# Kernel tuning notes

Hardware: AMD Instinct MI355X
Metric: run time of the kernel (lower is better)

Reference implementation:

```python
import jax, jax.numpy as jnp
import numpy as np

H = 256          # hidden_dim
B = 64           # molecules
M = 64           # atoms per molecule (equal-size molecules)
N = B * M        # total nodes
NE = 119         # element classes
NB = 5           # bond classes
EPS = 1e-5
OFF_I, OFF_J = np.where(~np.eye(M, dtype=bool))  # static off-diagonal pair order (i-major, j!=i)


def _gelu(x):
    return jax.nn.gelu(x, approximate=False)


def _ln(x, g, b):
    mu = jnp.mean(x, axis=-1, keepdims=True)
    var = jnp.mean((x - mu) ** 2, axis=-1, keepdims=True)
    return (x - mu) * jax.lax.rsqrt(var + EPS) * g + b


def _mlp(x, W1, b1, g, bn, W2, b2, W3, b3):
    x = _gelu(x @ W1 + b1)
    x = _ln(x, g, bn)
    x = _gelu(x @ W2 + b2)
    return x @ W3 + b3


def setup_inputs():
    key = jax.random.key(0)
    ks = jax.random.split(key, 16)
    s = 0.02
    def lin(k, fi, fo):
        return jax.random.normal(k, (fi, fo), jnp.float32) * s
    inp = {}
    inp["h"] = jax.random.normal(ks[0], (N, H), jnp.float32)
    inp["pos"] = jax.random.normal(ks[1], (N, 3), jnp.float32) * 3.0
    inp["edge_index"] = jax.random.randint(ks[2], (2, N * 8), 0, N)
    inp["batch"] = jnp.repeat(jnp.arange(B), M)
    # atom_predictor params
    inp["aW1"] = lin(ks[3], H, H); inp["ab1"] = jnp.zeros((H,))
    inp["ag"] = jnp.ones((H,)); inp["abn"] = jnp.zeros((H,))
    inp["aW2"] = lin(ks[4], H, H // 2); inp["ab2"] = jnp.zeros((H // 2,))
    inp["aW3"] = lin(ks[5], H // 2, NE); inp["ab3"] = jnp.zeros((NE,))
    # valency_predictor params
    inp["vW1"] = lin(ks[6], H + NE, H); inp["vb1"] = jnp.zeros((H,))
    inp["vg"] = jnp.ones((H,)); inp["vbn"] = jnp.zeros((H,))
    inp["vW2"] = lin(ks[7], H, H // 2); inp["vb2"] = jnp.zeros((H // 2,))
    inp["vW3"] = lin(ks[8], H // 2, 1); inp["vb3"] = jnp.zeros((1,))
    # bond_predictor params
    inp["bW1"] = lin(ks[9], 2 * H + 4, H); inp["bb1"] = jnp.zeros((H,))
    inp["bg"] = jnp.ones((H,)); inp["bbn"] = jnp.zeros((H,))
    inp["bW2"] = lin(ks[10], H, H // 2); inp["bb2"] = jnp.zeros((H // 2,))
    inp["bW3"] = lin(ks[11], H // 2, NB); inp["bb3"] = jnp.zeros((NB,))
    # chemical constant buffers (stand-ins for RDKit tables)
    mv = np.ones(NE, np.float32) * 4.0
    mv[[1, 9, 17, 35, 53]] = 1.0; mv[8] = 2.0; mv[7] = 3.0; mv[16] = 6.0; mv[15] = 5.0
    inp["max_valences"] = jnp.asarray(mv)
    cr = np.ones(NE, np.float32) * 1.5
    cr[1] = 0.31; cr[6] = 0.76; cr[7] = 0.71; cr[8] = 0.66; cr[9] = 0.57; cr[16] = 1.05
    inp["covalent_radii"] = jnp.asarray(cr)
    return inp


def _forward(h, pos, aW1, ab1, ag, abn, aW2, ab2, aW3, ab3,
             vW1, vb1, vg, vbn, vW2, vb2, vW3, vb3,
             bW1, bb1, bg, bbn, bW2, bb2, bW3, bb3,
             max_valences, covalent_radii):
    atom_logits = _mlp(h, aW1, ab1, ag, abn, aW2, ab2, aW3, ab3)        # [N,119]
    atom_probs = jax.nn.softmax(atom_logits, axis=-1)
    val = _mlp(jnp.concatenate([h, atom_probs], -1), vW1, vb1, vg, vbn, vW2, vb2, vW3, vb3)
    val = jax.nn.softplus(val)                                          # [N,1]
    pred = jnp.clip(jnp.argmax(atom_probs, -1), 0, 118)
    max_allowed = max_valences[pred]                                    # [N]
    # torch.min([N], [N,1]) broadcasts to [N,N] in the original -- reproduced faithfully
    valency_constrained = jnp.minimum(val[:, 0], max_allowed[:, None])  # [N,N]
    # vectorized pairwise bond prediction per molecule (equal-size molecules)
    hB = h.reshape(B, M, H)
    pB = pos.reshape(B, M, 3)
    probsB = atom_probs.reshape(B, M, NE)
    dist = jnp.linalg.norm(pB[:, :, None, :] - pB[:, None, :, :], axis=-1)  # [B,M,M]
    radii = covalent_radii[jnp.minimum(jnp.argmax(probsB, -1), 118)]        # [B,M]
    expected = radii[:, :, None] + radii[:, None, :]                        # [B,M,M]
    close = (dist < 3.0).astype(h.dtype)
    feats = jnp.concatenate([
        jnp.broadcast_to(hB[:, :, None, :], (B, M, M, H)),
        jnp.broadcast_to(hB[:, None, :, :], (B, M, M, H)),
        dist[..., None], expected[..., None],
        (dist / expected)[..., None], close[..., None],
    ], axis=-1)                                                             # [B,M,M,2H+4]
    logits = _mlp(feats, bW1, bb1, bg, bbn, bW2, bb2, bW3, bb3)             # [B,M,M,5]
    probs5 = jax.nn.softmax(logits, axis=-1)
    e0 = jnp.zeros((NB,), h.dtype).at[0].set(1.0)
    diag = jnp.eye(M, dtype=bool)[None, :, :, None]
    adjacency = jnp.where(diag, e0, probs5)                                 # [B,M,M,5]
    bond_logits = logits[:, OFF_I, OFF_J, :].reshape(B * M * (M - 1), NB)   # skip i==j, i-major order
    return (atom_logits, bond_logits, valency_constrained, adjacency)


def reference(h, pos, edge_index, batch, aW1, ab1, ag, abn, aW2, ab2, aW3, ab3,
              vW1, vb1, vg, vbn, vW2, vb2, vW3, vb3,
              bW1, bb1, bg, bbn, bW2, bb2, bW3, bb3, max_valences, covalent_radii):
    # edge_index is unused by the original forward; batch is implicit in the [B,M] layout
    return _forward(h, pos, aW1, ab1, ag, abn, aW2, ab2, aW3, ab3,
                    vW1, vb1, vg, vbn, vW2, vb2, vW3, vb3,
                    bW1, bb1, bg, bbn, bW2, bb2, bW3, bb3,
                    max_valences, covalent_radii)
```

## Files before the change

kernel.cpp:

```cpp
#include <hip/hip_runtime.h>
#include <math.h>

#define NN   4096
#define HH   256
#define NEC  119
#define NBC  5
#define NMOL 64
#define MAT  64

#define OFF_ATOM   0
#define SZ_ATOM    (4096*119)
#define OFF_BOND   487424
#define SZ_BOND    (258048*5)
#define OFF_VALM   (487424+1290240)
#define SZ_VALM    (4096*4096)
#define OFF_ADJ    (1777664+16777216)

typedef short  bf16x8 __attribute__((ext_vector_type(8)));
typedef float  f32x4  __attribute__((ext_vector_type(4)));

__device__ __forceinline__ float gelu_f(float x) {
    float z = fabsf(x) * 0.70710678118654752f;
    float t = __builtin_amdgcn_rcpf(fmaf(0.3275911f, z, 1.0f));
    float p = t * fmaf(t, fmaf(t, fmaf(t, fmaf(t, 1.061405429f, -1.453152027f),
                                       1.421413741f), -0.284496736f), 0.254829592f);
    float er = fmaf(-p, __expf(-z * z), 1.0f);
    float s = copysignf(er, x);
    return 0.5f * x * (1.f + s);
}
__device__ __forceinline__ unsigned short f2bf(float x) {
    unsigned int u = __float_as_uint(x);
    unsigned int r = (u + 0x7fffu + ((u >> 16) & 1u)) >> 16;
    return (unsigned short)r;
}

__global__ __launch_bounds__(256) void k_front(
    const float* __restrict__ h,
    const float* __restrict__ aW1, const float* __restrict__ ab1,
    const float* __restrict__ ag,  const float* __restrict__ abn,
    const float* __restrict__ aW2, const float* __restrict__ ab2,
    const float* __restrict__ aW3, const float* __restrict__ ab3,
    const float* __restrict__ maxv, const float* __restrict__ covr,
    const float* __restrict__ vW1, const float* __restrict__ vb1,
    const float* __restrict__ vg,  const float* __restrict__ vbn,
    const float* __restrict__ vW2, const float* __restrict__ vb2,
    const float* __restrict__ vW3, const float* __restrict__ vb3,
    const float* __restrict__ bW1, const float* __restrict__ bb1,
    const float* __restrict__ bW2, const float* __restrict__ bW3,
    float* __restrict__ logits_out,
    float* __restrict__ ma, float* __restrict__ rad, float* __restrict__ val,
    float* __restrict__ P, float* __restrict__ Q,
    short* __restrict__ W2f, short* __restrict__ W3f)
{
    __shared__ float smem[7056];
    float (*hs)[376]   = (float(*)[376])smem;
    float (*z1)[256]   = (float(*)[256])(smem + 3008);
    float (*z2)[128]   = (float(*)[128])(smem + 5056);
    float (*llog)[120] = (float(*)[120])(smem + 6080);
    float (*redbuf)[2] = (float(*)[2])  (smem + 7040);

    const int t  = threadIdx.x;
    const int wv = t >> 6, ln = t & 63;

    if (blockIdx.x >= 512) {
        const int pb = blockIdx.x - 512;
        const int n0 = pb * 8;

        if (pb < 128) {
            const int id = pb * 256 + t;
            {
                const int e = id & 7, l = (id >> 3) & 63, ks = (id >> 9) & 7, ct = (id >> 12) & 7;
                const int k = ks * 32 + (l >> 4) * 8 + e;
                const int col = ct * 16 + (l & 15);
                W2f[id] = (short)f2bf(bW2[k * 128 + col]);
            }
            if (id < 2048) {
                const int e = id & 7, l = (id >> 3) & 63, ks = id >> 9;
                const int k = ks * 32 + (l >> 4) * 8 + e;
                const int col = l & 15;
                W3f[id] = (col < NBC) ? (short)f2bf(bW3[k * NBC + col]) : (short)0;
            }
        }

        float (*hq)[256] = (float(*)[256])smem;
        for (int idx = t; idx < 8 * 256; idx += 256)
            ((float*)hq)[idx] = h[(size_t)n0 * 256 + idx];
        __syncthreads();

        const int c = t;
        float accp[8], accq[8];
        float b1 = bb1[c];
        #pragma unroll
        for (int r = 0; r < 8; ++r) { accp[r] = b1; accq[r] = 0.f; }
        for (int k4 = 0; k4 < 64; ++k4) {
            const int k = k4 * 4;
            float p0 = bW1[(k + 0) * 256 + c];
            float p1 = bW1[(k + 1) * 256 + c];
            float p2 = bW1[(k + 2) * 256 + c];
            float p3 = bW1[(k + 3) * 256 + c];
            float q0 = bW1[(256 + k + 0) * 256 + c];
            float q1 = bW1[(256 + k + 1) * 256 + c];
            float q2 = bW1[(256 + k + 2) * 256 + c];
            float q3 = bW1[(256 + k + 3) * 256 + c];
            #pragma unroll
            for (int r = 0; r < 8; ++r) {
                float4 hv = *(const float4*)&hq[r][k];
                accp[r] = fmaf(hv.x, p0, accp[r]);
                accp[r] = fmaf(hv.y, p1, accp[r]);
                accp[r] = fmaf(hv.z, p2, accp[r]);
                accp[r] = fmaf(hv.w, p3, accp[r]);
                accq[r] = fmaf(hv.x, q0, accq[r]);
                accq[r] = fmaf(hv.y, q1, accq[r]);
                accq[r] = fmaf(hv.z, q2, accq[r]);
                accq[r] = fmaf(hv.w, q3, accq[r]);
            }
        }
        #pragma unroll
        for (int r = 0; r < 8; ++r) {
            P[(size_t)(n0 + r) * 256 + c] = accp[r];
            Q[(size_t)(n0 + r) * 256 + c] = accq[r];
        }
        return;
    }

    const int n0 = blockIdx.x * 8;

    for (int idx = t; idx < 8 * 256; idx += 256) {
        int r = idx >> 8, cc = idx & 255;
        hs[r][cc] = h[(size_t)(n0 + r) * 256 + cc];
    }
    if (t < 8) hs[t][375] = 0.f;
    __syncthreads();

    {
        const int c = t;
        float b1 = ab1[c];
        float acc[8];
        #pragma unroll
        for (int r = 0; r < 8; ++r) acc[r] = b1;
        for (int k4 = 0; k4 < 64; ++k4) {
            const int k = k4 * 4;
            float w0 = aW1[(k + 0) * 256 + c];
            float w1 = aW1[(k + 1) * 256 + c];
            float w2 = aW1[(k + 2) * 256 + c];
            float w3 = aW1[(k + 3) * 256 + c];
            #pragma unroll
            for (int r = 0; r < 8; ++r) {
                float4 hv = *(const float4*)&hs[r][k];
                acc[r] = fmaf(hv.x, w0, acc[r]);
                acc[r] = fmaf(hv.y, w1, acc[r]);
                acc[r] = fmaf(hv.z, w2, acc[r]);
                acc[r] = fmaf(hv.w, w3, acc[r]);
            }
        }
        #pragma unroll
        for (int r = 0; r < 8; ++r) z1[r][c] = gelu_f(acc[r]);
    }
    __syncthreads();

    for (int rr = 0; rr < 2; ++rr) {
        const int r = wv * 2 + rr;
        float s = 0.f, s2 = 0.f;
        #pragma unroll
        for (int q = 0; q < 4; ++q) {
            float v = z1[r][ln + q * 64];
            s += v; s2 = fmaf(v, v, s2);
        }
        #pragma unroll
        for (int m = 32; m >= 1; m >>= 1) {
            s  += __shfl_xor(s,  m, 64);
            s2 += __shfl_xor(s2, m, 64);
        }
        if (ln == 0) {
            float mu  = s * (1.f / 256.f);
            float var = s2 * (1.f / 256.f) - mu * mu;
            redbuf[r][0] = mu;
            redbuf[r][1] = rsqrtf(var + 1e-5f);
        }
    }
    __syncthreads();
    {
        const int c = t;
        float g = ag[c], b = abn[c];
        #pragma unroll
        for (int r = 0; r < 8; ++r)
            z1[r][c] = (z1[r][c] - redbuf[r][0]) * redbuf[r][1] * g + b;
    }
    __syncthreads();

    {
        const int c2 = t & 127, kh = t >> 7;
        float acc2[8];
        #pragma unroll
        for (int r = 0; r < 8; ++r) acc2[r] = 0.f;
        const int kb = kh * 128;
        for (int k4 = 0; k4 < 32; ++k4) {
            const int k = kb + k4 * 4;
            float w0 = aW2[(k + 0) * 128 + c2];
            float w1 = aW2[(k + 1) * 128 + c2];
            float w2 = aW2[(k + 2) * 128 + c2];
            float w3 = aW2[(k + 3) * 128 + c2];
            #pragma unroll
            for (int r = 0; r < 8; ++r) {
                float4 zv = *(const float4*)&z1[r][k];
                acc2[r] = fmaf(zv.x, w0, acc2[r]);
                acc2[r] = fmaf(zv.y, w1, acc2[r]);
                acc2[r] = fmaf(zv.z, w2, acc2[r]);
                acc2[r] = fmaf(zv.w, w3, acc2[r]);
            }
        }
        if (kh == 1) {
            #pragma unroll
            for (int r = 0; r < 8; ++r) z2[r][c2] = acc2[r];
        }
        __syncthreads();
        if (kh == 0) {
            float b2 = ab2[c2];
            #pragma unroll
            for (int r = 0; r < 8; ++r)
                z2[r][c2] = gelu_f(acc2[r] + z2[r][c2] + b2);
        }
    }
    __syncthreads();

    if (t < NEC) {
        const int c = t;
        float b3 = ab3[c];
        float acc3[8];
        #pragma unroll
        for (int r = 0; r < 8; ++r) acc3[r] = b3;
        for (int k4 = 0; k4 < 32; ++k4) {
            const int k = k4 * 4;
            float w0 = aW3[(k + 0) * NEC + c];
            float w1 = aW3[(k + 1) * NEC + c];
            float w2 = aW3[(k + 2) * NEC + c];
            float w3 = aW3[(k + 3) * NEC + c];
            #pragma unroll
            for (int r = 0; r < 8; ++r) {
                float4 zv = *(const float4*)&z2[r][k];
                acc3[r] = fmaf(zv.x, w0, acc3[r]);
                acc3[r] = fmaf(zv.y, w1, acc3[r]);
                acc3[r] = fmaf(zv.z, w2, acc3[r]);
                acc3[r] = fmaf(zv.w, w3, acc3[r]);
            }
        }
        #pragma unroll
        for (int r = 0; r < 8; ++r) {
            llog[r][c] = acc3[r];
            logits_out[(size_t)(n0 + r) * NEC + c] = acc3[r];
        }
    }
    __syncthreads();

    for (int rr = 0; rr < 2; ++rr) {
        const int r = wv * 2 + rr;
        float v1 = llog[r][ln];
        float v2 = (ln + 64 < NEC) ? llog[r][ln + 64] : -1e30f;
        float mx; int mi;
        if (v2 > v1) { mx = v2; mi = ln + 64; } else { mx = v1; mi = ln; }
        #pragma unroll
        for (int m = 32; m >= 1; m >>= 1) {
            float ov = __shfl_xor(mx, m, 64);
            int   oi = __shfl_xor(mi, m, 64);
            if (ov > mx || (ov == mx && oi < mi)) { mx = ov; mi = oi; }
        }
        float e1 = __expf(v1 - mx);
        float e2 = (ln + 64 < NEC) ? __expf(v2 - mx) : 0.f;
        float s = e1 + e2;
        #pragma unroll
        for (int m = 32; m >= 1; m >>= 1) s += __shfl_xor(s, m, 64);
        float inv = __builtin_amdgcn_rcpf(s);
        hs[r][256 + ln] = e1 * inv;
        if (ln + 64 < NEC) hs[r][256 + ln + 64] = e2 * inv;
        if (ln == 0) {
            ma[n0 + r]  = maxv[mi];
            rad[n0 + r] = covr[mi];
        }
    }
    __syncthreads();

    {
        const int c = t;
        float b1 = vb1[c];
        float acc[8];
        #pragma unroll
        for (int r = 0; r < 8; ++r) acc[r] = b1;
        for (int k4 = 0; k4 < 93; ++k4) {
            const int k = k4 * 4;
            float w0 = vW1[(k + 0) * 256 + c];
            float w1 = vW1[(k + 1) * 256 + c];
            float w2 = vW1[(k + 2) * 256 + c];
            float w3 = vW1[(k + 3) * 256 + c];
            #pragma unroll
            for (int r = 0; r < 8; ++r) {
                float4 hv = *(const float4*)&hs[r][k];
                acc[r] = fmaf(hv.x, w0, acc[r]);
                acc[r] = fmaf(hv.y, w1, acc[r]);
                acc[r] = fmaf(hv.z, w2, acc[r]);
                acc[r] = fmaf(hv.w, w3, acc[r]);
            }
        }
        {
            float w0 = vW1[372 * 256 + c];
            float w1 = vW1[373 * 256 + c];
            float w2 = vW1[374 * 256 + c];
            #pragma unroll
            for (int r = 0; r < 8; ++r) {
                acc[r] = fmaf(hs[r][372], w0, acc[r]);
                acc[r] = fmaf(hs[r][373], w1, acc[r]);
                acc[r] = fmaf(hs[r][374], w2, acc[r]);
            }
        }
        #pragma unroll
        for (int r = 0; r < 8; ++r) z1[r][c] = gelu_f(acc[r]);
    }
    __syncthreads();

    for (int rr = 0; rr < 2; ++rr) {
        const int r = wv * 2 + rr;
        float s = 0.f, s2 = 0.f;
        #pragma unroll
        for (int q = 0; q < 4; ++q) {
            float v = z1[r][ln + q * 64];
            s += v; s2 = fmaf(v, v, s2);
        }
        #pragma unroll
        for (int m = 32; m >= 1; m >>= 1) {
            s  += __shfl_xor(s,  m, 64);
            s2 += __shfl_xor(s2, m, 64);
        }
        if (ln == 0) {
            float mu  = s * (1.f / 256.f);
            float var = s2 * (1.f / 256.f) - mu * mu;
            redbuf[r][0] = mu;
            redbuf[r][1] = rsqrtf(var + 1e-5f);
        }
    }
    __syncthreads();
    {
        const int c = t;
        float g = vg[c], b = vbn[c];
        #pragma unroll
        for (int r = 0; r < 8; ++r)
            z1[r][c] = (z1[r][c] - redbuf[r][0]) * redbuf[r][1] * g + b;
    }
    __syncthreads();

    {
        const int c2 = t & 127, kh = t >> 7;
        float acc2[8];
        #pragma unroll
        for (int r = 0; r < 8; ++r) acc2[r] = 0.f;
        const int kb = kh * 128;
        for (int k4 = 0; k4 < 32; ++k4) {
            const int k = kb + k4 * 4;
            float w0 = vW2[(k + 0) * 128 + c2];
            float w1 = vW2[(k + 1) * 128 + c2];
            float w2 = vW2[(k + 2) * 128 + c2];
            float w3 = vW2[(k + 3) * 128 + c2];
            #pragma unroll
            for (int r = 0; r < 8; ++r) {
                float4 zv = *(const float4*)&z1[r][k];
                acc2[r] = fmaf(zv.x, w0, acc2[r]);
                acc2[r] = fmaf(zv.y, w1, acc2[r]);
                acc2[r] = fmaf(zv.z, w2, acc2[r]);
                acc2[r] = fmaf(zv.w, w3, acc2[r]);
            }
        }
        if (kh == 1) {
            #pragma unroll
            for (int r = 0; r < 8; ++r) z2[r][c2] = acc2[r];
        }
        __syncthreads();
        if (kh == 0) {
            float b2 = vb2[c2];
            #pragma unroll
            for (int r = 0; r < 8; ++r)
                z2[r][c2] = gelu_f(acc2[r] + z2[r][c2] + b2);
        }
    }
    __syncthreads();

    for (int rr = 0; rr < 2; ++rr) {
        const int r = wv * 2 + rr;
        float p = fmaf(z2[r][ln], vW3[ln], z2[r][ln + 64] * vW3[ln + 64]);
        #pragma unroll
        for (int m = 32; m >= 1; m >>= 1) p += __shfl_xor(p, m, 64);
        if (ln == 0) {
            float x = p + vb3[0];
            val[n0 + r] = (x > 15.f) ? x : log1pf(expf(x));
        }
    }
}

__global__ __launch_bounds__(256) void k_back(
    const float* __restrict__ pos, const float* __restrict__ rad,
    const float* __restrict__ P, const float* __restrict__ Q,
    const float* __restrict__ bW1,
    const float* __restrict__ bg, const float* __restrict__ bbn,
    const float* __restrict__ bb2,
    const short* __restrict__ W2f, const short* __restrict__ W3f,
    const float* __restrict__ bb3,
    const float* __restrict__ val, const float* __restrict__ ma,
    float* __restrict__ bond_logits, float* __restrict__ adjacency,
    float* __restrict__ valmat)
{
    __shared__ float posr[64][4];
    __shared__ float bb2s[128];
    __shared__ unsigned short Xs[64 * 256];
    __shared__ float Ls[64][5];
    unsigned short* Ys = Xs;

    const int t  = threadIdx.x;

    if (blockIdx.x >= 4096) {
        const int i0 = (blockIdx.x - 4096) * 8;
        const float4* v4 = (const float4*)val;
        for (int rr = 0; rr < 8; ++rr) {
            const int i = i0 + rr;
            const float mi = ma[i];
            float4* o4 = (float4*)(valmat + (size_t)i * 4096);
            for (int j = t; j < 1024; j += 256) {
                float4 v = v4[j];
                float4 r;
                r.x = fminf(v.x, mi); r.y = fminf(v.y, mi);
                r.z = fminf(v.z, mi); r.w = fminf(v.w, mi);
                o4[j] = r;
            }
        }
        return;
    }

    const int bi = blockIdx.x;
    const int b  = bi >> 6, i = bi & 63;
    const int wv = t >> 6, ln = t & 63;
    const int node0 = b * 64;

    if (t < 64) {
        int n = node0 + t;
        posr[t][0] = pos[n * 3 + 0];
        posr[t][1] = pos[n * 3 + 1];
        posr[t][2] = pos[n * 3 + 2];
        posr[t][3] = rad[n];
    }
    if (t >= 128 && t < 256) bb2s[t - 128] = bb2[t - 128];
    __syncthreads();

    {
        const int c0 = ln * 4;
        const size_t nodei = (size_t)(node0 + i);
        float4 Pi  = *(const float4*)(P + nodei * 256 + c0);
        float4 w0  = *(const float4*)(bW1 + (size_t)512 * 256 + c0);
        float4 w1  = *(const float4*)(bW1 + (size_t)513 * 256 + c0);
        float4 w2  = *(const float4*)(bW1 + (size_t)514 * 256 + c0);
        float4 w3  = *(const float4*)(bW1 + (size_t)515 * 256 + c0);
        float4 gam = *(const float4*)(bg  + c0);
        float4 bet = *(const float4*)(bbn + c0);
        const float xi = posr[i][0], yi = posr[i][1], zi = posr[i][2], ri = posr[i][3];

        #pragma unroll 2
        for (int jj = 0; jj < 16; ++jj) {
            const int j = wv * 16 + jj;
            float dx = xi - posr[j][0];
            float dy = yi - posr[j][1];
            float dz = zi - posr[j][2];
            float dist = sqrtf(fmaf(dx, dx, fmaf(dy, dy, dz * dz)));
            float expd = ri + posr[j][3];
            float ratio = dist * __builtin_amdgcn_rcpf(expd);
            float close = (dist < 3.f) ? 1.f : 0.f;
            float4 qv = *(const float4*)(Q + (size_t)(node0 + j) * 256 + c0);

            float g0 = Pi.x + qv.x;
            g0 = fmaf(w0.x, dist, g0); g0 = fmaf(w1.x, expd, g0);
            g0 = fmaf(w2.x, ratio, g0); g0 = fmaf(w3.x, close, g0);
            float g1 = Pi.y + qv.y;
            g1 = fmaf(w0.y, dist, g1); g1 = fmaf(w1.y, expd, g1);
            g1 = fmaf(w2.y, ratio, g1); g1 = fmaf(w3.y, close, g1);
            float g2 = Pi.z + qv.z;
            g2 = fmaf(w0.z, dist, g2); g2 = fmaf(w1.z, expd, g2);
            g2 = fmaf(w2.z, ratio, g2); g2 = fmaf(w3.z, close, g2);
            float g3 = Pi.w + qv.w;
            g3 = fmaf(w0.w, dist, g3); g3 = fmaf(w1.w, expd, g3);
            g3 = fmaf(w2.w, ratio, g3); g3 = fmaf(w3.w, close, g3);
            g0 = gelu_f(g0); g1 = gelu_f(g1); g2 = gelu_f(g2); g3 = gelu_f(g3);

            float s  = g0 + g1 + g2 + g3;
            float s2 = fmaf(g0, g0, fmaf(g1, g1, fmaf(g2, g2, g3 * g3)));
            #pragma unroll
            for (int m = 32; m >= 1; m >>= 1) {
                s  += __shfl_xor(s,  m, 64);
                s2 += __shfl_xor(s2, m, 64);
            }
            float mu   = s * (1.f / 256.f);
            float rstd = rsqrtf(s2 * (1.f / 256.f) - mu * mu + 1e-5f);

            ushort4 u;
            u.x = f2bf((g0 - mu) * rstd * gam.x + bet.x);
            u.y = f2bf((g1 - mu) * rstd * gam.y + bet.y);
            u.z = f2bf((g2 - mu) * rstd * gam.z + bet.z);
            u.w = f2bf((g3 - mu) * rstd * gam.w + bet.w);
            const int chunk = ln >> 1;
            const int off   = j * 512 + ((chunk ^ (j & 7)) << 4) + ((ln & 1) << 3);
            *(ushort4*)((char*)Xs + off) = u;
        }
    }
    __syncthreads();

    {
        const int lrow = ln & 15, lk = ln >> 4;
        f32x4 acc[4][2];
        #pragma unroll
        for (int jt = 0; jt < 4; ++jt)
            #pragma unroll
            for (int c2 = 0; c2 < 2; ++c2)
                acc[jt][c2] = (f32x4){0.f, 0.f, 0.f, 0.f};

        #pragma unroll
        for (int ks = 0; ks < 8; ++ks) {
            bf16x8 bfr0 = *(const bf16x8*)(W2f + (((size_t)(2 * wv + 0) * 8 + ks) * 64 + ln) * 8);
            bf16x8 bfr1 = *(const bf16x8*)(W2f + (((size_t)(2 * wv + 1) * 8 + ks) * 64 + ln) * 8);
            #pragma unroll
            for (int jt = 0; jt < 4; ++jt) {
                const int row   = jt * 16 + lrow;
                const int chunk = ks * 4 + lk;
                const int off   = row * 512 + ((chunk ^ (row & 7)) << 4);
                bf16x8 afr = *(const bf16x8*)((char*)Xs + off);
                acc[jt][0] = __builtin_amdgcn_mfma_f32_16x16x32_bf16(afr, bfr0, acc[jt][0], 0, 0, 0);
                acc[jt][1] = __builtin_amdgcn_mfma_f32_16x16x32_bf16(afr, bfr1, acc[jt][1], 0, 0, 0);
            }
        }
        __syncthreads();

        #pragma unroll
        for (int jt = 0; jt < 4; ++jt) {
            #pragma unroll
            for (int c2 = 0; c2 < 2; ++c2) {
                const int col = (2 * wv + c2) * 16 + lrow;
                const float bb = bb2s[col];
                #pragma unroll
                for (int r = 0; r < 4; ++r) {
                    const int row = jt * 16 + lk * 4 + r;
                    float y = gelu_f(acc[jt][c2][r] + bb);
                    const int chunk = col >> 3;
                    const int off = row * 256 + ((chunk ^ (row & 7)) << 4) + ((col & 7) << 1);
                    *(unsigned short*)((char*)Ys + off) = f2bf(y);
                }
            }
        }
    }
    __syncthreads();

    {
        const int lrow = ln & 15, lk = ln >> 4;
        f32x4 acc3 = (f32x4){0.f, 0.f, 0.f, 0.f};
        #pragma unroll
        for (int ks = 0; ks < 4; ++ks) {
            bf16x8 bfr = *(const bf16x8*)(W3f + ((size_t)(ks * 64 + ln)) * 8);
            const int row   = wv * 16 + lrow;
            const int chunk = ks * 4 + lk;
            const int off   = row * 256 + ((chunk ^ (row & 7)) << 4);
            bf16x8 afr = *(const bf16x8*)((char*)Ys + off);
            acc3 = __builtin_amdgcn_mfma_f32_16x16x32_bf16(afr, bfr, acc3, 0, 0, 0);
        }
        if (lrow < NBC) {
            #pragma unroll
            for (int r = 0; r < 4; ++r)
                Ls[wv * 16 + lk * 4 + r][lrow] = acc3[r];
        }
    }
    __syncthreads();

    const size_t adjbase  = (size_t)bi * 64 * 5;
    const size_t bondbase = ((size_t)b * 4032 + (size_t)i * 63) * 5;
    const float b30 = bb3[0], b31 = bb3[1], b32 = bb3[2], b33 = bb3[3], b34 = bb3[4];
    for (int u = t; u < 320; u += 256) {
        const int j = u / 5, o = u - (u / 5) * 5;
        float l0 = Ls[j][0] + b30, l1 = Ls[j][1] + b31, l2 = Ls[j][2] + b32;
        float l3 = Ls[j][3] + b33, l4 = Ls[j][4] + b34;
        float mx = fmaxf(fmaxf(fmaxf(l0, l1), fmaxf(l2, l3)), l4);
        float e0 = __expf(l0 - mx), e1 = __expf(l1 - mx), e2 = __expf(l2 - mx);
        float e3 = __expf(l3 - mx), e4 = __expf(l4 - mx);
        float inv = __builtin_amdgcn_rcpf(e0 + e1 + e2 + e3 + e4);
        float lo = (o == 0) ? l0 : (o == 1) ? l1 : (o == 2) ? l2 : (o == 3) ? l3 : l4;
        float po = ((o == 0) ? e0 : (o == 1) ? e1 : (o == 2) ? e2 : (o == 3) ? e3 : e4) * inv;
        adjacency[adjbase + u] = (j == i) ? ((o == 0) ? 1.f : 0.f) : po;
        if (j != i) {
            const int jj = j - (j > i ? 1 : 0);
            bond_logits[bondbase + (size_t)jj * 5 + o] = lo;
        }
    }
}

extern "C" void kernel_launch(void* const* d_in, const int* in_sizes, int n_in,
                              void* d_out, int out_size, void* d_ws, size_t ws_size,
                              hipStream_t stream)
{
    (void)in_sizes; (void)n_in; (void)out_size; (void)ws_size;
    const float* h   = (const float*)d_in[0];
    const float* pos = (const float*)d_in[1];
    const float* aW1 = (const float*)d_in[4];
    const float* ab1 = (const float*)d_in[5];
    const float* ag  = (const float*)d_in[6];
    const float* abn = (const float*)d_in[7];
    const float* aW2 = (const float*)d_in[8];
    const float* ab2 = (const float*)d_in[9];
    const float* aW3 = (const float*)d_in[10];
    const float* ab3 = (const float*)d_in[11];
    const float* vW1 = (const float*)d_in[12];
    const float* vb1 = (const float*)d_in[13];
    const float* vg  = (const float*)d_in[14];
    const float* vbn = (const float*)d_in[15];
    const float* vW2 = (const float*)d_in[16];
    const float* vb2 = (const float*)d_in[17];
    const float* vW3 = (const float*)d_in[18];
    const float* vb3 = (const float*)d_in[19];
    const float* bW1 = (const float*)d_in[20];
    const float* bb1 = (const float*)d_in[21];
    const float* bg  = (const float*)d_in[22];
    const float* bbn = (const float*)d_in[23];
    const float* bW2 = (const float*)d_in[24];
    const float* bb2 = (const float*)d_in[25];
    const float* bW3 = (const float*)d_in[26];
    const float* bb3 = (const float*)d_in[27];
    const float* mv  = (const float*)d_in[28];
    const float* cr  = (const float*)d_in[29];

    float* out = (float*)d_out;
    float* atom_logits = out + OFF_ATOM;
    float* bond_logits = out + OFF_BOND;
    float* valmat      = out + OFF_VALM;
    float* adjacency   = out + OFF_ADJ;

    float* ws    = (float*)d_ws;
    float* ma    = ws;
    float* rad   = ws + 4096;
    float* val   = ws + 8192;
    float* Pp    = ws + 12288;
    float* Qq    = ws + 1060864;
    short* W2f   = (short*)(ws + 2109440);
    short* W3f   = (short*)(ws + 2125824);

    k_front<<<1024, 256, 0, stream>>>(h,
        aW1, ab1, ag, abn, aW2, ab2, aW3, ab3, mv, cr,
        vW1, vb1, vg, vbn, vW2, vb2, vW3, vb3,
        bW1, bb1, bW2, bW3,
        atom_logits, ma, rad, val, Pp, Qq, W2f, W3f);
    k_back<<<4608, 256, 0, stream>>>(pos, rad, Pp, Qq, bW1, bg, bbn,
                                     bb2, W2f, W3f, bb3, val, ma,
                                     bond_logits, adjacency, valmat);
}
```

Before: 334.0 us.

## Fold bond LayerNorm affine into W2 and build MFMA fragments in registers

The bond path now algebraically folds the LayerNorm mean/rstd and beta into the second linear layer, using precomputed u = gamma·W2 and v = beta·W2 + b2. This lets each lane build its bf16 A-fragments directly in registers from gelu(P+Q+geometry)·gamma, which removes the 64x256 LDS staging buffer and two block barriers. k_front is reshaped to 4 rows per block with twice as many blocks and a smaller shared footprint, and launch bounds are added on both kernels. The trade-offs are bf16 rounding of unnormalized activations, which shifts numerics slightly, higher register pressure (8 accumulators plus 8 fragments), and per-lane global Q reads.

```diff
diff --git a/kernel.cpp b/kernel.cpp
--- a/kernel.cpp
+++ b/kernel.cpp
@@ -34,7 +34,7 @@
     return (unsigned short)r;
 }
 
-__global__ __launch_bounds__(256) void k_front(
+__global__ __launch_bounds__(256, 8) void k_front(
     const float* __restrict__ h,
     const float* __restrict__ aW1, const float* __restrict__ ab1,
     const float* __restrict__ ag,  const float* __restrict__ abn,
@@ -47,24 +47,27 @@
     const float* __restrict__ vW3, const float* __restrict__ vb3,
     const float* __restrict__ bW1, const float* __restrict__ bb1,
     const float* __restrict__ bW2, const float* __restrict__ bW3,
+    const float* __restrict__ bg,  const float* __restrict__ bbn,
+    const float* __restrict__ bb2,
     float* __restrict__ logits_out,
     float* __restrict__ ma, float* __restrict__ rad, float* __restrict__ val,
     float* __restrict__ P, float* __restrict__ Q,
-    short* __restrict__ W2f, short* __restrict__ W3f)
+    short* __restrict__ W2f, short* __restrict__ W3f,
+    float* __restrict__ uu, float* __restrict__ vvb)
 {
-    __shared__ float smem[7056];
+    __shared__ float smem[3532];
     float (*hs)[376]   = (float(*)[376])smem;
-    float (*z1)[256]   = (float(*)[256])(smem + 3008);
-    float (*z2)[128]   = (float(*)[128])(smem + 5056);
-    float (*llog)[120] = (float(*)[120])(smem + 6080);
-    float (*redbuf)[2] = (float(*)[2])  (smem + 7040);
+    float (*z1)[256]   = (float(*)[256])(smem + 1504);
+    float (*z2)[128]   = (float(*)[128])(smem + 2528);
+    float (*llog)[120] = (float(*)[120])(smem + 3040);
+    float (*redbuf)[2] = (float(*)[2])  (smem + 3520);
 
     const int t  = threadIdx.x;
     const int wv = t >> 6, ln = t & 63;
 
-    if (blockIdx.x >= 512) {
-        const int pb = blockIdx.x - 512;
-        const int n0 = pb * 8;
+    if (blockIdx.x >= 1024) {
+        const int pb = blockIdx.x - 1024;
+        const int n0 = pb * 4;
 
         if (pb < 128) {
             const int id = pb * 256 + t;
@@ -80,18 +83,29 @@
                 const int col = l & 15;
                 W3f[id] = (col < NBC) ? (short)f2bf(bW3[k * NBC + col]) : (short)0;
             }
+        } else if (pb == 128) {
+            if (t < 128) {
+                float ua = 0.f, va = 0.f;
+                for (int c = 0; c < 256; ++c) {
+                    float w = bW2[c * 128 + t];
+                    ua = fmaf(bg[c],  w, ua);
+                    va = fmaf(bbn[c], w, va);
+                }
+                uu[t]  = ua;
+                vvb[t] = va + bb2[t];
+            }
         }
 
         float (*hq)[256] = (float(*)[256])smem;
-        for (int idx = t; idx < 8 * 256; idx += 256)
+        for (int idx = t; idx < 4 * 256; idx += 256)
             ((float*)hq)[idx] = h[(size_t)n0 * 256 + idx];
         __syncthreads();
 
         const int c = t;
-        float accp[8], accq[8];
+        float accp[4], accq[4];
         float b1 = bb1[c];
         #pragma unroll
-        for (int r = 0; r < 8; ++r) { accp[r] = b1; accq[r] = 0.f; }
+        for (int r = 0; r < 4; ++r) { accp[r] = b1; accq[r] = 0.f; }
         for (int k4 = 0; k4 < 64; ++k4) {
             const int k = k4 * 4;
             float p0 = bW1[(k + 0) * 256 + c];
@@ -103,7 +117,7 @@
             float q2 = bW1[(256 + k + 2) * 256 + c];
             float q3 = bW1[(256 + k + 3) * 256 + c];
             #pragma unroll
-            for (int r = 0; r < 8; ++r) {
+            for (int r = 0; r < 4; ++r) {
                 float4 hv = *(const float4*)&hq[r][k];
                 accp[r] = fmaf(hv.x, p0, accp[r]);
                 accp[r] = fmaf(hv.y, p1, accp[r]);
@@ -116,28 +130,28 @@
             }
         }
         #pragma unroll
-        for (int r = 0; r < 8; ++r) {
+        for (int r = 0; r < 4; ++r) {
             P[(size_t)(n0 + r) * 256 + c] = accp[r];
             Q[(size_t)(n0 + r) * 256 + c] = accq[r];
         }
         return;
     }
 
-    const int n0 = blockIdx.x * 8;
-
-    for (int idx = t; idx < 8 * 256; idx += 256) {
+    const int n0 = blockIdx.x * 4;
+
+    for (int idx = t; idx < 4 * 256; idx += 256) {
         int r = idx >> 8, cc = idx & 255;
         hs[r][cc] = h[(size_t)(n0 + r) * 256 + cc];
     }
-    if (t < 8) hs[t][375] = 0.f;
+    if (t < 4) hs[t][375] = 0.f;
     __syncthreads();
 
     {
         const int c = t;
         float b1 = ab1[c];
-        float acc[8];
-        #pragma unroll
-        for (int r = 0; r < 8; ++r) acc[r] = b1;
+        float acc[4];
+        #pragma unroll
+        for (int r = 0; r < 4; ++r) acc[r] = b1;
         for (int k4 = 0; k4 < 64; ++k4) {
             const int k = k4 * 4;
             float w0 = aW1[(k + 0) * 256 + c];
@@ -145,7 +159,7 @@
             float w2 = aW1[(k + 2) * 256 + c];
             float w3 = aW1[(k + 3) * 256 + c];
             #pragma unroll
-            for (int r = 0; r < 8; ++r) {
+            for (int r = 0; r < 4; ++r) {
                 float4 hv = *(const float4*)&hs[r][k];
                 acc[r] = fmaf(hv.x, w0, acc[r]);
                 acc[r] = fmaf(hv.y, w1, acc[r]);
@@ -154,12 +168,12 @@
             }
         }
         #pragma unroll
-        for (int r = 0; r < 8; ++r) z1[r][c] = gelu_f(acc[r]);
-    }
-    __syncthreads();
-
-    for (int rr = 0; rr < 2; ++rr) {
-        const int r = wv * 2 + rr;
+        for (int r = 0; r < 4; ++r) z1[r][c] = gelu_f(acc[r]);
+    }
+    __syncthreads();
+
+    {
+        const int r = wv;
         float s = 0.f, s2 = 0.f;
         #pragma unroll
         for (int q = 0; q < 4; ++q) {
@@ -183,16 +197,16 @@
         const int c = t;
         float g = ag[c], b = abn[c];
         #pragma unroll
-        for (int r = 0; r < 8; ++r)
+        for (int r = 0; r < 4; ++r)
             z1[r][c] = (z1[r][c] - redbuf[r][0]) * redbuf[r][1] * g + b;
     }
     __syncthreads();
 
     {
         const int c2 = t & 127, kh = t >> 7;
-        float acc2[8];
-        #pragma unroll
-        for (int r = 0; r < 8; ++r) acc2[r] = 0.f;
+        float acc2[4];
+        #pragma unroll
+        for (int r = 0; r < 4; ++r) acc2[r] = 0.f;
         const int kb = kh * 128;
         for (int k4 = 0; k4 < 32; ++k4) {
             const int k = kb + k4 * 4;
@@ -201,7 +215,7 @@
             float w2 = aW2[(k + 2) * 128 + c2];
             float w3 = aW2[(k + 3) * 128 + c2];
             #pragma unroll
-            for (int r = 0; r < 8; ++r) {
+            for (int r = 0; r < 4; ++r) {
                 float4 zv = *(const float4*)&z1[r][k];
                 acc2[r] = fmaf(zv.x, w0, acc2[r]);
                 acc2[r] = fmaf(zv.y, w1, acc2[r]);
@@ -211,13 +225,13 @@
         }
         if (kh == 1) {
             #pragma unroll
-            for (int r = 0; r < 8; ++r) z2[r][c2] = acc2[r];
+            for (int r = 0; r < 4; ++r) z2[r][c2] = acc2[r];
         }
         __syncthreads();
         if (kh == 0) {
             float b2 = ab2[c2];
             #pragma unroll
-            for (int r = 0; r < 8; ++r)
+            for (int r = 0; r < 4; ++r)
                 z2[r][c2] = gelu_f(acc2[r] + z2[r][c2] + b2);
         }
     }
@@ -226,9 +240,9 @@
     if (t < NEC) {
         const int c = t;
         float b3 = ab3[c];
-        float acc3[8];
-        #pragma unroll
-        for (int r = 0; r < 8; ++r) acc3[r] = b3;
+        float acc3[4];
+        #pragma unroll
+        for (int r = 0; r < 4; ++r) acc3[r] = b3;
         for (int k4 = 0; k4 < 32; ++k4) {
             const int k = k4 * 4;
             float w0 = aW3[(k + 0) * NEC + c];
@@ -236,7 +250,7 @@
             float w2 = aW3[(k + 2) * NEC + c];
             float w3 = aW3[(k + 3) * NEC + c];
             #pragma unroll
-            for (int r = 0; r < 8; ++r) {
+            for (int r = 0; r < 4; ++r) {
                 float4 zv = *(const float4*)&z2[r][k];
                 acc3[r] = fmaf(zv.x, w0, acc3[r]);
                 acc3[r] = fmaf(zv.y, w1, acc3[r]);
@@ -245,15 +259,15 @@
             }
         }
         #pragma unroll
-        for (int r = 0; r < 8; ++r) {
+        for (int r = 0; r < 4; ++r) {
             llog[r][c] = acc3[r];
             logits_out[(size_t)(n0 + r) * NEC + c] = acc3[r];
         }
     }
     __syncthreads();
 
-    for (int rr = 0; rr < 2; ++rr) {
-        const int r = wv * 2 + rr;
+    {
+        const int r = wv;
         float v1 = llog[r][ln];
         float v2 = (ln + 64 < NEC) ? llog[r][ln + 64] : -1e30f;
         float mx; int mi;
@@ -282,9 +296,9 @@
     {
         const int c = t;
         float b1 = vb1[c];
-        float acc[8];
-        #pragma unroll
-        for (int r = 0; r < 8; ++r) acc[r] = b1;
+        float acc[4];
+        #pragma unroll
+        for (int r = 0; r < 4; ++r) acc[r] = b1;
         for (int k4 = 0; k4 < 93; ++k4) {
             const int k = k4 * 4;
             float w0 = vW1[(k + 0) * 256 + c];
@@ -292,7 +306,7 @@
             float w2 = vW1[(k + 2) * 256 + c];
             float w3 = vW1[(k + 3) * 256 + c];
             #pragma unroll
-            for (int r = 0; r < 8; ++r) {
+            for (int r = 0; r < 4; ++r) {
                 float4 hv = *(const float4*)&hs[r][k];
                 acc[r] = fmaf(hv.x, w0, acc[r]);
                 acc[r] = fmaf(hv.y, w1, acc[r]);
@@ -305,19 +319,19 @@
             float w1 = vW1[373 * 256 + c];
             float w2 = vW1[374 * 256 + c];
             #pragma unroll
-            for (int r = 0; r < 8; ++r) {
+            for (int r = 0; r < 4; ++r) {
                 acc[r] = fmaf(hs[r][372], w0, acc[r]);
                 acc[r] = fmaf(hs[r][373], w1, acc[r]);
                 acc[r] = fmaf(hs[r][374], w2, acc[r]);
             }
         }
         #pragma unroll
-        for (int r = 0; r < 8; ++r) z1[r][c] = gelu_f(acc[r]);
-    }
-    __syncthreads();
-
-    for (int rr = 0; rr < 2; ++rr) {
-        const int r = wv * 2 + rr;
+        for (int r = 0; r < 4; ++r) z1[r][c] = gelu_f(acc[r]);
+    }
+    __syncthreads();
+
+    {
+        const int r = wv;
         float s = 0.f, s2 = 0.f;
         #pragma unroll
         for (int q = 0; q < 4; ++q) {
@@ -341,16 +355,16 @@
         const int c = t;
         float g = vg[c], b = vbn[c];
         #pragma unroll
-        for (int r = 0; r < 8; ++r)
+        for (int r = 0; r < 4; ++r)
             z1[r][c] = (z1[r][c] - redbuf[r][0]) * redbuf[r][1] * g + b;
     }
     __syncthreads();
 
     {
         const int c2 = t & 127, kh = t >> 7;
-        float acc2[8];
-        #pragma unroll
-        for (int r = 0; r < 8; ++r) acc2[r] = 0.f;
+        float acc2[4];
+        #pragma unroll
+        for (int r = 0; r < 4; ++r) acc2[r] = 0.f;
         const int kb = kh * 128;
         for (int k4 = 0; k4 < 32; ++k4) {
             const int k = kb + k4 * 4;
@@ -359,7 +373,7 @@
             float w2 = vW2[(k + 2) * 128 + c2];
             float w3 = vW2[(k + 3) * 128 + c2];
             #pragma unroll
-            for (int r = 0; r < 8; ++r) {
+            for (int r = 0; r < 4; ++r) {
                 float4 zv = *(const float4*)&z1[r][k];
                 acc2[r] = fmaf(zv.x, w0, acc2[r]);
                 acc2[r] = fmaf(zv.y, w1, acc2[r]);
@@ -369,20 +383,20 @@
         }
         if (kh == 1) {
             #pragma unroll
-            for (int r = 0; r < 8; ++r) z2[r][c2] = acc2[r];
+            for (int r = 0; r < 4; ++r) z2[r][c2] = acc2[r];
         }
         __syncthreads();
         if (kh == 0) {
             float b2 = vb2[c2];
             #pragma unroll
-            for (int r = 0; r < 8; ++r)
+            for (int r = 0; r < 4; ++r)
                 z2[r][c2] = gelu_f(acc2[r] + z2[r][c2] + b2);
         }
     }
     __syncthreads();
 
-    for (int rr = 0; rr < 2; ++rr) {
-        const int r = wv * 2 + rr;
+    {
+        const int r = wv;
         float p = fmaf(z2[r][ln], vW3[ln], z2[r][ln + 64] * vW3[ln + 64]);
         #pragma unroll
         for (int m = 32; m >= 1; m >>= 1) p += __shfl_xor(p, m, 64);
@@ -393,23 +407,24 @@
     }
 }
 
-__global__ __launch_bounds__(256) void k_back(
+__global__ __launch_bounds__(256, 4) void k_back(
     const float* __restrict__ pos, const float* __restrict__ rad,
     const float* __restrict__ P, const float* __restrict__ Q,
-    const float* __restrict__ bW1,
-    const float* __restrict__ bg, const float* __restrict__ bbn,
-    const float* __restrict__ bb2,
+    const float* __restrict__ bW1, const float* __restrict__ bg,
     const short* __restrict__ W2f, const short* __restrict__ W3f,
     const float* __restrict__ bb3,
+    const float* __restrict__ uu, const float* __restrict__ vvb,
     const float* __restrict__ val, const float* __restrict__ ma,
     float* __restrict__ bond_logits, float* __restrict__ adjacency,
     float* __restrict__ valmat)
 {
     __shared__ float posr[64][4];
-    __shared__ float bb2s[128];
-    __shared__ unsigned short Xs[64 * 256];
+    __shared__ float Pis[256];
+    __shared__ float wst0[256], wst1[256], wst2[256], wst3[256];
+    __shared__ float gams[256];
+    __shared__ float us_[128], vbs[128];
+    __shared__ unsigned short Ys[64 * 128];
     __shared__ float Ls[64][5];
-    unsigned short* Ys = Xs;
 
     const int t  = threadIdx.x;
 
@@ -434,7 +449,9 @@
     const int bi = blockIdx.x;
     const int b  = bi >> 6, i = bi & 63;
     const int wv = t >> 6, ln = t & 63;
+    const int lr = ln & 15, kg = ln >> 4;
     const int node0 = b * 64;
+    const int j = wv * 16 + lr;
 
     if (t < 64) {
         int n = node0 + t;
@@ -443,149 +460,125 @@
         posr[t][2] = pos[n * 3 + 2];
         posr[t][3] = rad[n];
     }
-    if (t >= 128 && t < 256) bb2s[t - 128] = bb2[t - 128];
-    __syncthreads();
-
-    {
-        const int c0 = ln * 4;
-        const size_t nodei = (size_t)(node0 + i);
-        float4 Pi  = *(const float4*)(P + nodei * 256 + c0);
-        float4 w0  = *(const float4*)(bW1 + (size_t)512 * 256 + c0);
-        float4 w1  = *(const float4*)(bW1 + (size_t)513 * 256 + c0);
-        float4 w2  = *(const float4*)(bW1 + (size_t)514 * 256 + c0);
-        float4 w3  = *(const float4*)(bW1 + (size_t)515 * 256 + c0);
-        float4 gam = *(const float4*)(bg  + c0);
-        float4 bet = *(const float4*)(bbn + c0);
-        const float xi = posr[i][0], yi = posr[i][1], zi = posr[i][2], ri = posr[i][3];
-
-        #pragma unroll 2
-        for (int jj = 0; jj < 16; ++jj) {
-            const int j = wv * 16 + jj;
-            float dx = xi - posr[j][0];
-            float dy = yi - posr[j][1];
-            float dz = zi - posr[j][2];
-            float dist = sqrtf(fmaf(dx, dx, fmaf(dy, dy, dz * dz)));
-            float expd = ri + posr[j][3];
-            float ratio = dist * __builtin_amdgcn_rcpf(expd);
-            float close = (dist < 3.f) ? 1.f : 0.f;
-            float4 qv = *(const float4*)(Q + (size_t)(node0 + j) * 256 + c0);
-
-            float g0 = Pi.x + qv.x;
-            g0 = fmaf(w0.x, dist, g0); g0 = fmaf(w1.x, expd, g0);
-            g0 = fmaf(w2.x, ratio, g0); g0 = fmaf(w3.x, close, g0);
-            float g1 = Pi.y + qv.y;
-            g1 = fmaf(w0.y, dist, g1); g1 = fmaf(w1.y, expd, g1);
-            g1 = fmaf(w2.y, ratio, g1); g1 = fmaf(w3.y, close, g1);
-            float g2 = Pi.z + qv.z;
-            g2 = fmaf(w0.z, dist, g2); g2 = fmaf(w1.z, expd, g2);
-            g2 = fmaf(w2.z, ratio, g2); g2 = fmaf(w3.z, close, g2);
-            float g3 = Pi.w + qv.w;
-            g3 = fmaf(w0.w, dist, g3); g3 = fmaf(w1.w, expd, g3);
-            g3 = fmaf(w2.w, ratio, g3); g3 = fmaf(w3.w, close, g3);
-            g0 = gelu_f(g0); g1 = gelu_f(g1); g2 = gelu_f(g2); g3 = gelu_f(g3);
-
-            float s  = g0 + g1 + g2 + g3;
-            float s2 = fmaf(g0, g0, fmaf(g1, g1, fmaf(g2, g2, g3 * g3)));
-            #pragma unroll
-            for (int m = 32; m >= 1; m >>= 1) {
-                s  += __shfl_xor(s,  m, 64);
-                s2 += __shfl_xor(s2, m, 64);
-            }
-            float mu   = s * (1.f / 256.f);
-            float rstd = rsqrtf(s2 * (1.f / 256.f) - mu * mu + 1e-5f);
-
-            ushort4 u;
-            u.x = f2bf((g0 - mu) * rstd * gam.x + bet.x);
-            u.y = f2bf((g1 - mu) * rstd * gam.y + bet.y);
-            u.z = f2bf((g2 - mu) * rstd * gam.z + bet.z);
-            u.w = f2bf((g3 - mu) * rstd * gam.w + bet.w);
-            const int chunk = ln >> 1;
-            const int off   = j * 512 + ((chunk ^ (j & 7)) << 4) + ((ln & 1) << 3);
-            *(ushort4*)((char*)Xs + off) = u;
-        }
-    }
-    __syncthreads();
-
-    {
-        const int lrow = ln & 15, lk = ln >> 4;
-        f32x4 acc[4][2];
-        #pragma unroll
-        for (int jt = 0; jt < 4; ++jt)
-            #pragma unroll
-            for (int c2 = 0; c2 < 2; ++c2)
-                acc[jt][c2] = (f32x4){0.f, 0.f, 0.f, 0.f};
-
-        #pragma unroll
-        for (int ks = 0; ks < 8; ++ks) {
-            bf16x8 bfr0 = *(const bf16x8*)(W2f + (((size_t)(2 * wv + 0) * 8 + ks) * 64 + ln) * 8);
-            bf16x8 bfr1 = *(const bf16x8*)(W2f + (((size_t)(2 * wv + 1) * 8 + ks) * 64 + ln) * 8);
-            #pragma unroll
-            for (int jt = 0; jt < 4; ++jt) {
-                const int row   = jt * 16 + lrow;
-                const int chunk = ks * 4 + lk;
-                const int off   = row * 512 + ((chunk ^ (row & 7)) << 4);
-                bf16x8 afr = *(const bf16x8*)((char*)Xs + off);
-                acc[jt][0] = __builtin_amdgcn_mfma_f32_16x16x32_bf16(afr, bfr0, acc[jt][0], 0, 0, 0);
-                acc[jt][1] = __builtin_amdgcn_mfma_f32_16x16x32_bf16(afr, bfr1, acc[jt][1], 0, 0, 0);
-            }
-        }
-        __syncthreads();
-
-        #pragma unroll
-        for (int jt = 0; jt < 4; ++jt) {
-            #pragma unroll
-            for (int c2 = 0; c2 < 2; ++c2) {
-                const int col = (2 * wv + c2) * 16 + lrow;
-                const float bb = bb2s[col];
-                #pragma unroll
-                for (int r = 0; r < 4; ++r) {
-                    const int row = jt * 16 + lk * 4 + r;
-                    float y = gelu_f(acc[jt][c2][r] + bb);
-                    const int chunk = col >> 3;
-                    const int off = row * 256 + ((chunk ^ (row & 7)) << 4) + ((col & 7) << 1);
-                    *(unsigned short*)((char*)Ys + off) = f2bf(y);
-                }
-            }
-        }
-    }
-    __syncthreads();
-
-    {
-        const int lrow = ln & 15, lk = ln >> 4;
+    Pis[t]  = P[(size_t)(node0 + i) * 256 + t];
+    wst0[t] = bW1[(size_t)512 * 256 + t];
+    wst1[t] = bW1[(size_t)513 * 256 + t];
+    wst2[t] = bW1[(size_t)514 * 256 + t];
+    wst3[t] = bW1[(size_t)515 * 256 + t];
+    gams[t] = bg[t];
+    if (t < 128) { us_[t] = uu[t]; vbs[t] = vvb[t]; }
+    __syncthreads();
+
+    float dx = posr[i][0] - posr[j][0];
+    float dy = posr[i][1] - posr[j][1];
+    float dz = posr[i][2] - posr[j][2];
+    float dist  = sqrtf(fmaf(dx, dx, fmaf(dy, dy, dz * dz)));
+    float expd  = posr[i][3] + posr[j][3];
+    float ratio = dist * __builtin_amdgcn_rcpf(expd);
+    float close = (dist < 3.f) ? 1.f : 0.f;
+
+    float s = 0.f, s2 = 0.f;
+    bf16x8 afr[8];
+    const float* Qrow = Q + (size_t)(node0 + j) * 256;
+    #pragma unroll
+    for (int ks = 0; ks < 8; ++ks) {
+        const int base = ks * 32 + kg * 8;
+        float4 Pa  = *(const float4*)&Pis[base],  Pb  = *(const float4*)&Pis[base + 4];
+        float4 Qa  = *(const float4*)(Qrow + base), Qb = *(const float4*)(Qrow + base + 4);
+        float4 w0a = *(const float4*)&wst0[base], w0b = *(const float4*)&wst0[base + 4];
+        float4 w1a = *(const float4*)&wst1[base], w1b = *(const float4*)&wst1[base + 4];
+        float4 w2a = *(const float4*)&wst2[base], w2b = *(const float4*)&wst2[base + 4];
+        float4 w3a = *(const float4*)&wst3[base], w3b = *(const float4*)&wst3[base + 4];
+        float4 ga  = *(const float4*)&gams[base], gb  = *(const float4*)&gams[base + 4];
+        float g, xg;
+        #define LANECH(P_, Q_, W0_, W1_, W2_, W3_, G_, EI) \
+            g = P_ + Q_; g = fmaf(W0_, dist, g); g = fmaf(W1_, expd, g); \
+            g = fmaf(W2_, ratio, g); g = fmaf(W3_, close, g); g = gelu_f(g); \
+            s += g; s2 = fmaf(g, g, s2); xg = g * G_; afr[ks][EI] = (short)f2bf(xg);
+        LANECH(Pa.x, Qa.x, w0a.x, w1a.x, w2a.x, w3a.x, ga.x, 0)
+        LANECH(Pa.y, Qa.y, w0a.y, w1a.y, w2a.y, w3a.y, ga.y, 1)
+        LANECH(Pa.z, Qa.z, w0a.z, w1a.z, w2a.z, w3a.z, ga.z, 2)
+        LANECH(Pa.w, Qa.w, w0a.w, w1a.w, w2a.w, w3a.w, ga.w, 3)
+        LANECH(Pb.x, Qb.x, w0b.x, w1b.x, w2b.x, w3b.x, gb.x, 4)
+        LANECH(Pb.y, Qb.y, w0b.y, w1b.y, w2b.y, w3b.y, gb.y, 5)
+        LANECH(Pb.z, Qb.z, w0b.z, w1b.z, w2b.z, w3b.z, gb.z, 6)
+        LANECH(Pb.w, Qb.w, w0b.w, w1b.w, w2b.w, w3b.w, gb.w, 7)
+        #undef LANECH
+    }
+    s  += __shfl_xor(s,  16, 64);  s  += __shfl_xor(s,  32, 64);
+    s2 += __shfl_xor(s2, 16, 64);  s2 += __shfl_xor(s2, 32, 64);
+    const float mu   = s * (1.f / 256.f);
+    const float rstd = rsqrtf(s2 * (1.f / 256.f) - mu * mu + 1e-5f);
+
+    f32x4 acc[8];
+    #pragma unroll
+    for (int ct = 0; ct < 8; ++ct) acc[ct] = (f32x4){0.f, 0.f, 0.f, 0.f};
+    #pragma unroll
+    for (int ks = 0; ks < 8; ++ks) {
+        #pragma unroll
+        for (int ct = 0; ct < 8; ++ct) {
+            bf16x8 bfr = *(const bf16x8*)(W2f + (((size_t)(ct * 8 + ks)) * 64 + ln) * 8);
+            acc[ct] = __builtin_amdgcn_mfma_f32_16x16x32_bf16(afr[ks], bfr, acc[ct], 0, 0, 0);
+        }
+    }
+
+    float rst[4], rm[4];
+    #pragma unroll
+    for (int r = 0; r < 4; ++r) {
+        float sr = __shfl(rstd, kg * 4 + r, 64);
+        float mr = __shfl(mu,   kg * 4 + r, 64);
+        rst[r] = sr; rm[r] = sr * mr;
+    }
+    #pragma unroll
+    for (int ct = 0; ct < 8; ++ct) {
+        const int col = ct * 16 + lr;
+        const float ucv = us_[col], vcv = vbs[col];
+        #pragma unroll
+        for (int r = 0; r < 4; ++r) {
+            float y = fmaf(rst[r], acc[ct][r], fmaf(-rm[r], ucv, vcv));
+            y = gelu_f(y);
+            const int row = wv * 16 + kg * 4 + r;
+            const int chunk = col >> 3;
+            const int off = row * 256 + ((chunk ^ (row & 7)) << 4) + ((col & 7) << 1);
+            *(unsigned short*)((char*)Ys + off) = f2bf(y);
+        }
+    }
+
+    {
         f32x4 acc3 = (f32x4){0.f, 0.f, 0.f, 0.f};
         #pragma unroll
         for (int ks = 0; ks < 4; ++ks) {
             bf16x8 bfr = *(const bf16x8*)(W3f + ((size_t)(ks * 64 + ln)) * 8);
-            const int row   = wv * 16 + lrow;
-            const int chunk = ks * 4 + lk;
+            const int row   = wv * 16 + lr;
+            const int chunk = ks * 4 + kg;
             const int off   = row * 256 + ((chunk ^ (row & 7)) << 4);
-            bf16x8 afr = *(const bf16x8*)((char*)Ys + off);
-            acc3 = __builtin_amdgcn_mfma_f32_16x16x32_bf16(afr, bfr, acc3, 0, 0, 0);
-        }
-        if (lrow < NBC) {
+            bf16x8 afr2 = *(const bf16x8*)((char*)Ys + off);
+            acc3 = __builtin_amdgcn_mfma_f32_16x16x32_bf16(afr2, bfr, acc3, 0, 0, 0);
+        }
+        if (lr < NBC) {
             #pragma unroll
             for (int r = 0; r < 4; ++r)
-                Ls[wv * 16 + lk * 4 + r][lrow] = acc3[r];
-        }
-    }
-    __syncthreads();
+                Ls[wv * 16 + kg * 4 + r][lr] = acc3[r];
+        }
+    }
 
     const size_t adjbase  = (size_t)bi * 64 * 5;
     const size_t bondbase = ((size_t)b * 4032 + (size_t)i * 63) * 5;
     const float b30 = bb3[0], b31 = bb3[1], b32 = bb3[2], b33 = bb3[3], b34 = bb3[4];
-    for (int u = t; u < 320; u += 256) {
-        const int j = u / 5, o = u - (u / 5) * 5;
-        float l0 = Ls[j][0] + b30, l1 = Ls[j][1] + b31, l2 = Ls[j][2] + b32;
-        float l3 = Ls[j][3] + b33, l4 = Ls[j][4] + b34;
+    for (int u = ln; u < 80; u += 64) {
+        const int jl = u / 5, o = u - jl * 5;
+        const int j2 = wv * 16 + jl;
+        float l0 = Ls[j2][0] + b30, l1 = Ls[j2][1] + b31, l2 = Ls[j2][2] + b32;
+        float l3 = Ls[j2][3] + b33, l4 = Ls[j2][4] + b34;
         float mx = fmaxf(fmaxf(fmaxf(l0, l1), fmaxf(l2, l3)), l4);
         float e0 = __expf(l0 - mx), e1 = __expf(l1 - mx), e2 = __expf(l2 - mx);
         float e3 = __expf(l3 - mx), e4 = __expf(l4 - mx);
         float inv = __builtin_amdgcn_rcpf(e0 + e1 + e2 + e3 + e4);
         float lo = (o == 0) ? l0 : (o == 1) ? l1 : (o == 2) ? l2 : (o == 3) ? l3 : l4;
         float po = ((o == 0) ? e0 : (o == 1) ? e1 : (o == 2) ? e2 : (o == 3) ? e3 : e4) * inv;
-        adjacency[adjbase + u] = (j == i) ? ((o == 0) ? 1.f : 0.f) : po;
-        if (j != i) {
-            const int jj = j - (j > i ? 1 : 0);
+        adjacency[adjbase + (size_t)j2 * 5 + o] = (j2 == i) ? ((o == 0) ? 1.f : 0.f) : po;
+        if (j2 != i) {
+            const int jj = j2 - (j2 > i ? 1 : 0);
             bond_logits[bondbase + (size_t)jj * 5 + o] = lo;
         }
     }
@@ -639,13 +632,15 @@
     float* Qq    = ws + 1060864;
     short* W2f   = (short*)(ws + 2109440);
     short* W3f   = (short*)(ws + 2125824);
-
-    k_front<<<1024, 256, 0, stream>>>(h,
+    float* uu    = ws + 2126848;
+    float* vvb   = ws + 2126976;
+
+    k_front<<<2048, 256, 0, stream>>>(h,
         aW1, ab1, ag, abn, aW2, ab2, aW3, ab3, mv, cr,
         vW1, vb1, vg, vbn, vW2, vb2, vW3, vb3,
-        bW1, bb1, bW2, bW3,
-        atom_logits, ma, rad, val, Pp, Qq, W2f, W3f);
-    k_back<<<4608, 256, 0, stream>>>(pos, rad, Pp, Qq, bW1, bg, bbn,
-                                     bb2, W2f, W3f, bb3, val, ma,
+        bW1, bb1, bW2, bW3, bg, bbn, bb2,
+        atom_logits, ma, rad, val, Pp, Qq, W2f, W3f, uu, vvb);
+    k_back<<<4608, 256, 0, stream>>>(pos, rad, Pp, Qq, bW1, bg,
+                                     W2f, W3f, bb3, uu, vvb, val, ma,
                                      bond_logits, adjacency, valmat);
 }
```

After: 356.9 us. +6.9%, slower.
